# Kernel optimization log

Measured on AMD Instinct MI355X. Metric: run time of the kernel, lower is better.

## Reference

```python
import jax, jax.numpy as jnp
import numpy as np

N_NODES = 32768
N_EDGES = 131072
BATCH = 512
SEQ_LEN = 1000
VOCAB = 26  # vocab_size=25 + 1 padding row
EMB = 128


def _bn(x, g, b):
    # BatchNorm1d forward with batch statistics (training-mode math), eps=1e-5
    m = x.mean(0)
    v = x.var(0)
    return g * (x - m) * jax.lax.rsqrt(v + 1e-5) + b


def _gcn(x, src, dst, W, b, n):
    deg = 1.0 + jax.ops.segment_sum(jnp.ones(src.shape[0], x.dtype), dst, num_segments=n)
    dis = jax.lax.rsqrt(deg)
    xw = x @ W
    msg = xw[src] * (dis[src] * dis[dst])[:, None]
    agg = jax.ops.segment_sum(msg, dst, num_segments=n) + xw * (dis * dis)[:, None]
    return agg + b


def _conv1d(x, k, b, pad):
    # x: [B, C_in, L], k: [C_out, C_in, K]
    y = jax.lax.conv_general_dilated(x, k, (1,), [(pad, pad)],
                                     dimension_numbers=('NCH', 'OIH', 'NCH'))
    return y + b[None, :, None]


def setup_inputs() -> dict:
    key = jax.random.key(0)
    ks = jax.random.split(key, 32)
    f = lambda i, shape, s=0.1: (jax.random.normal(ks[i], shape, dtype=jnp.float32) * s)
    inp = {
        'x': jax.random.normal(ks[0], (N_NODES, 5), dtype=jnp.float32),
        'edge_index': jax.random.randint(ks[1], (2, N_EDGES), 0, N_NODES, dtype=jnp.int32),
        'batch': jnp.sort(jax.random.randint(ks[2], (N_NODES,), 0, BATCH, dtype=jnp.int32)),
        'protein_seq': jax.random.randint(ks[3], (BATCH, SEQ_LEN), 0, VOCAB, dtype=jnp.int32),
        # GCN weights
        'W1': f(4, (5, 64)), 'b1': f(5, (64,)),
        'g1': jnp.ones((64,)), 'bt1': jnp.zeros((64,)),
        'W2': f(6, (64, 128)), 'b2': f(7, (128,)),
        'g2': jnp.ones((128,)), 'bt2': jnp.zeros((128,)),
        'W3': f(8, (128, 128)), 'b3': f(9, (128,)),
        'g3': jnp.ones((128,)), 'bt3': jnp.zeros((128,)),
        # protein embedding (row 0 = padding_idx, zeroed)
        'emb': f(10, (VOCAB, EMB)).at[0].set(0.0),
        # protein convs
        'ck1': f(11, (32, 128, 4)), 'cb1': f(12, (32,)),
        'ck2': f(13, (64, 32, 6)), 'cb2': f(14, (64,)),
        'ck3': f(15, (96, 64, 8)), 'cb3': f(16, (96,)),
        'fw1': f(17, (224, 512)), 'fb1': f(18, (512,)),
        'fw2': f(19, (512, 256)), 'fb2': f(20, (256,)),
        'fw3': f(21, (256, 1)), 'fb3': f(22, (1,)),
    }
    return inp


def reference(x, edge_index, batch, protein_seq,
              W1, b1, g1, bt1, W2, b2, g2, bt2, W3, b3, g3, bt3,
              emb, ck1, cb1, ck2, cb2, ck3, cb3,
              fw1, fb1, fw2, fb2, fw3, fb3):
    src, dst = edge_index[0], edge_index[1]
    relu = jax.nn.relu
    # Drug GNN encoder
    h = relu(_bn(_gcn(x, src, dst, W1, b1, N_NODES), g1, bt1))
    h = relu(_bn(_gcn(h, src, dst, W2, b2, N_NODES), g2, bt2))
    h = relu(_bn(_gcn(h, src, dst, W3, b3, N_NODES), g3, bt3))
    cnt = jax.ops.segment_sum(jnp.ones(N_NODES, h.dtype), batch, num_segments=BATCH)
    drug_emb = jax.ops.segment_sum(h, batch, num_segments=BATCH) / jnp.maximum(cnt, 1.0)[:, None]
    # Protein CNN encoder
    e = emb[protein_seq]                    # [B, L, 128]
    p = jnp.transpose(e, (0, 2, 1))         # [B, 128, L]
    p = relu(_conv1d(p, ck1, cb1, 1))       # [B, 32, 999]
    p = relu(_conv1d(p, ck2, cb2, 2))       # [B, 64, 998]
    p = relu(_conv1d(p, ck3, cb3, 3))       # [B, 96, 997]
    prot_emb = p.max(axis=2)                # [B, 96]
    c = jnp.concatenate([drug_emb, prot_emb], axis=1)  # [B, 224]
    c = relu(c @ fw1 + fb1)
    c = relu(c @ fw2 + fb2)
    out = (c @ fw3 + fb3)[:, 0]             # [B]
    return out
```

## Files before the change

### kernel.cpp

```cpp
#include <hip/hip_runtime.h>

#define NN 32768
#define NE 131072
#define NB 512
#define SL 1000

using bf16x8 = __attribute__((ext_vector_type(8))) short;
using f32x4  = __attribute__((ext_vector_type(4))) float;

static __device__ __forceinline__ unsigned short f2b(float f) {
  union { float f; unsigned u; } x; x.f = f;
  unsigned r = x.u + 0x7fffu + ((x.u >> 16) & 1u);
  return (unsigned short)(r >> 16);
}

static __device__ __forceinline__ void bn_from_raw(float sum, float ssq, float g, float b,
                                                   float& sc, float& sh) {
  float m = sum / 32768.f;
  float v = ssq / 32768.f - m * m;
  sc = g * rsqrtf(v + 1e-5f);
  sh = b - m * sc;
}

__global__ void k_degprep(const int* __restrict__ dst, int* __restrict__ degi,
                          const float* __restrict__ emb, const float* __restrict__ ck1,
                          const float* __restrict__ ck2, const float* __restrict__ ck3,
                          unsigned short* __restrict__ emb_bf, unsigned short* __restrict__ wt1,
                          unsigned short* __restrict__ wt2, unsigned short* __restrict__ wt3,
                          float* __restrict__ e1) {
  int gid = blockIdx.x * 256 + threadIdx.x;
  atomicAdd(&degi[dst[gid]], 1);
  int idx = gid;
  if (idx < 3328) {
    emb_bf[idx] = f2b(emb[idx]);
  } else if (idx < 3328 + 16384) {
    int i = idx - 3328;
    int kt = i >> 12, co = (i >> 7) & 31, ci = i & 127;
    wt1[i] = f2b(ck1[co * 512 + ci * 4 + kt]);
  } else if (idx < 3328 + 16384 + 12288) {
    int i = idx - 3328 - 16384;
    int kt = i >> 11, co = (i >> 5) & 63, ci = i & 31;
    wt2[i] = f2b(ck2[co * 192 + ci * 6 + kt]);
  } else if (idx < 3328 + 16384 + 12288 + 49152) {
    int i = idx - 3328 - 16384 - 12288;
    int kt = i / 6144, co = (i >> 6) % 96, ci = i & 63;
    wt3[i] = f2b(ck3[co * 512 + ci * 8 + kt]);
  } else if (idx < 3328 + 16384 + 12288 + 49152 + 3328) {
    int i = idx - 81152;
    int t = i >> 7, kt = (i >> 5) & 3, co = i & 31;
    const float* er = emb + t * 128;
    float s = 0.f;
#pragma unroll 4
    for (int ci = 0; ci < 128; ++ci) s += er[ci] * ck1[co * 512 + ci * 4 + kt];
    e1[i] = s;
  }
}

__global__ void k_scan(const int* __restrict__ degi, int* __restrict__ base,
                       int* __restrict__ cursor, float* __restrict__ dis) {
  __shared__ int part[1024];
  int tid = threadIdx.x;
  int v[32];
  int s = 0;
  int lo = tid * 32;
#pragma unroll
  for (int i = 0; i < 32; ++i) { v[i] = degi[lo + i]; s += v[i]; }
  part[tid] = s;
  __syncthreads();
  for (int off = 1; off < 1024; off <<= 1) {
    int val = (tid >= off) ? part[tid - off] : 0;
    __syncthreads();
    part[tid] += val;
    __syncthreads();
  }
  int run = (tid > 0) ? part[tid - 1] : 0;
#pragma unroll
  for (int i = 0; i < 32; ++i) {
    base[lo + i] = run;
    cursor[lo + i] = run;
    dis[lo + i] = rsqrtf(1.0f + (float)v[i]);
    run += v[i];
  }
  if (tid == 1023) base[NN] = run;
}

__global__ void k_fill(const int* __restrict__ src, const int* __restrict__ dst,
                       int* __restrict__ cursor, unsigned short* __restrict__ csr_src, int E) {
  int e = blockIdx.x * 256 + threadIdx.x;
  if (e < E) {
    int d = dst[e];
    int pos = atomicAdd(&cursor[d], 1);
    csr_src[pos] = (unsigned short)src[e];
  }
}

__launch_bounds__(256)
__global__ void k_gfc1s(const float* __restrict__ x, const float* __restrict__ dis,
                        const int* __restrict__ base, const unsigned short* __restrict__ csr_src,
                        const float* __restrict__ W1, float* __restrict__ out,
                        float* __restrict__ st) {
  __shared__ float sW[5][64];
  __shared__ float a5[256][6];
  __shared__ float red[16][64];
  int tid = threadIdx.x;
  for (int i = tid; i < 320; i += 256) sW[i >> 6][i & 63] = W1[i];
  int n = blockIdx.x * 256 + tid;
  float dn = dis[n];
  float s2 = dn * dn;
  const float* xn = x + (long)n * 5;
  float a0 = xn[0] * s2, a1 = xn[1] * s2, a2 = xn[2] * s2, a3 = xn[3] * s2, a4 = xn[4] * s2;
  int b0 = base[n], b1 = base[n + 1];
  int sNext = (b0 < b1) ? csr_src[b0] : 0;
  for (int j = b0; j < b1; ++j) {
    int s = sNext;
    if (j + 1 < b1) sNext = csr_src[j + 1];
    float coef = dis[s] * dn;
    const float* xs = x + (long)s * 5;
    a0 += xs[0] * coef; a1 += xs[1] * coef; a2 += xs[2] * coef;
    a3 += xs[3] * coef; a4 += xs[4] * coef;
  }
  a5[tid][0] = a0; a5[tid][1] = a1; a5[tid][2] = a2; a5[tid][3] = a3; a5[tid][4] = a4;
  __syncthreads();
  int co = (tid & 15) * 4, strip = tid >> 4;
  float4 s4 = {0.f, 0.f, 0.f, 0.f}, ss4 = {0.f, 0.f, 0.f, 0.f};
  for (int i = 0; i < 16; ++i) {
    int nl = strip * 16 + i;
    long nn = (long)blockIdx.x * 256 + nl;
    float4 acc = {0.f, 0.f, 0.f, 0.f};
#pragma unroll
    for (int ci = 0; ci < 5; ++ci) {
      float av = a5[nl][ci];
      acc.x += av * sW[ci][co];     acc.y += av * sW[ci][co + 1];
      acc.z += av * sW[ci][co + 2]; acc.w += av * sW[ci][co + 3];
    }
    *(float4*)&out[nn * 64 + co] = acc;
    s4.x += acc.x; s4.y += acc.y; s4.z += acc.z; s4.w += acc.w;
    ss4.x += acc.x * acc.x; ss4.y += acc.y * acc.y;
    ss4.z += acc.z * acc.z; ss4.w += acc.w * acc.w;
  }
  *(float4*)&red[strip][co] = s4;
  __syncthreads();
  if (tid < 64) {
    float t = 0.f;
#pragma unroll
    for (int s = 0; s < 16; ++s) t += red[s][tid];
    atomicAdd(&st[tid], t);
  }
  __syncthreads();
  *(float4*)&red[strip][co] = ss4;
  __syncthreads();
  if (tid < 64) {
    float t = 0.f;
#pragma unroll
    for (int s = 0; s < 16; ++s) t += red[s][tid];
    atomicAdd(&st[64 + tid], t);
  }
}

template<int C>
__launch_bounds__(256)
__global__ void k_gbngather(const float* __restrict__ in, const float* __restrict__ dis,
                            const int* __restrict__ base, const unsigned short* __restrict__ csr_src,
                            const float* __restrict__ st, const float* __restrict__ g,
                            const float* __restrict__ bt, float* __restrict__ out) {
  constexpr int TPN = C / 4;
  int t = blockIdx.x * 256 + threadIdx.x;
  int n = t / TPN;
  int c = (t % TPN) * 4;
  float4 sum4 = *(const float4*)&st[c];
  float4 ssq4 = *(const float4*)&st[C + c];
  float4 gg = *(const float4*)&g[c];
  float4 bb = *(const float4*)&bt[c];
  float4 sc4, sh4;
  bn_from_raw(sum4.x, ssq4.x, gg.x, bb.x, sc4.x, sh4.x);
  bn_from_raw(sum4.y, ssq4.y, gg.y, bb.y, sc4.y, sh4.y);
  bn_from_raw(sum4.z, ssq4.z, gg.z, bb.z, sc4.z, sh4.z);
  bn_from_raw(sum4.w, ssq4.w, gg.w, bb.w, sc4.w, sh4.w);
  float dn = dis[n];
  float s2 = dn * dn;
  float4 a = *(const float4*)&in[(long)n * C + c];
  float4 acc;
  acc.x = fmaxf(a.x * sc4.x + sh4.x, 0.f) * s2;
  acc.y = fmaxf(a.y * sc4.y + sh4.y, 0.f) * s2;
  acc.z = fmaxf(a.z * sc4.z + sh4.z, 0.f) * s2;
  acc.w = fmaxf(a.w * sc4.w + sh4.w, 0.f) * s2;
  int b0 = base[n], b1 = base[n + 1];
  int sNext = (b0 < b1) ? csr_src[b0] : 0;
  for (int j = b0; j < b1; ++j) {
    int s = sNext;
    if (j + 1 < b1) sNext = csr_src[j + 1];
    float coef = dis[s] * dn;
    float4 vv = *(const float4*)&in[(long)s * C + c];
    acc.x += fmaxf(vv.x * sc4.x + sh4.x, 0.f) * coef;
    acc.y += fmaxf(vv.y * sc4.y + sh4.y, 0.f) * coef;
    acc.z += fmaxf(vv.z * sc4.z + sh4.z, 0.f) * coef;
    acc.w += fmaxf(vv.w * sc4.w + sh4.w, 0.f) * coef;
  }
  *(float4*)&out[(long)n * C + c] = acc;
}

template<int C_OUT, int K, int TN, bool RELU, bool BIAS, bool STATS>
__launch_bounds__(256)
__global__ void k_fc4(const float* __restrict__ in, const float* __restrict__ W,
                      const float* __restrict__ bias, float* __restrict__ out,
                      float* __restrict__ st, int N) {
  constexpr int CO4 = C_OUT / 4;
  constexpr int GPB = 256 / CO4;
  int g = blockIdx.x * GPB + threadIdx.x / CO4;
  long n0 = (long)g * TN;
  if (!STATS && n0 >= N) return;
  int co = (threadIdx.x % CO4) * 4;
  float4 acc[TN];
  float4 b4 = {0.f, 0.f, 0.f, 0.f};
  if (BIAS) b4 = *(const float4*)&bias[co];
#pragma unroll
  for (int t = 0; t < TN; ++t) acc[t] = b4;
  for (int ci = 0; ci < K; ci += 4) {
    float4 w0 = *(const float4*)&W[(long)(ci + 0) * C_OUT + co];
    float4 w1 = *(const float4*)&W[(long)(ci + 1) * C_OUT + co];
    float4 w2 = *(const float4*)&W[(long)(ci + 2) * C_OUT + co];
    float4 w3 = *(const float4*)&W[(long)(ci + 3) * C_OUT + co];
#pragma unroll
    for (int t = 0; t < TN; ++t) {
      float4 a = *(const float4*)&in[(n0 + t) * K + ci];
      acc[t].x += a.x * w0.x; acc[t].y += a.x * w0.y; acc[t].z += a.x * w0.z; acc[t].w += a.x * w0.w;
      acc[t].x += a.y * w1.x; acc[t].y += a.y * w1.y; acc[t].z += a.y * w1.z; acc[t].w += a.y * w1.w;
      acc[t].x += a.z * w2.x; acc[t].y += a.z * w2.y; acc[t].z += a.z * w2.z; acc[t].w += a.z * w2.w;
      acc[t].x += a.w * w3.x; acc[t].y += a.w * w3.y; acc[t].z += a.w * w3.z; acc[t].w += a.w * w3.w;
    }
  }
  float4 s4 = {0.f, 0.f, 0.f, 0.f}, ss4 = {0.f, 0.f, 0.f, 0.f};
#pragma unroll
  for (int t = 0; t < TN; ++t) {
    float4 o = acc[t];
    if (RELU) {
      o.x = fmaxf(o.x, 0.f); o.y = fmaxf(o.y, 0.f);
      o.z = fmaxf(o.z, 0.f); o.w = fmaxf(o.w, 0.f);
    }
    *(float4*)&out[(n0 + t) * C_OUT + co] = o;
    if (STATS) {
      s4.x += o.x; s4.y += o.y; s4.z += o.z; s4.w += o.w;
      ss4.x += o.x * o.x; ss4.y += o.y * o.y;
      ss4.z += o.z * o.z; ss4.w += o.w * o.w;
    }
  }
  if (STATS) {
    __shared__ float red2[GPB][C_OUT];
    int grp = threadIdx.x / CO4;
    *(float4*)&red2[grp][co] = s4;
    __syncthreads();
    if (threadIdx.x < C_OUT) {
      float t = 0.f;
#pragma unroll
      for (int s = 0; s < GPB; ++s) t += red2[s][threadIdx.x];
      atomicAdd(&st[threadIdx.x], t);
    }
    __syncthreads();
    *(float4*)&red2[grp][co] = ss4;
    __syncthreads();
    if (threadIdx.x < C_OUT) {
      float t = 0.f;
#pragma unroll
      for (int s = 0; s < GPB; ++s) t += red2[s][threadIdx.x];
      atomicAdd(&st[C_OUT + threadIdx.x], t);
    }
  }
}

__launch_bounds__(256)
__global__ void k_reg(const float* __restrict__ cbuf,
                      const float* __restrict__ fw1, const float* __restrict__ fb1,
                      const float* __restrict__ fw2, const float* __restrict__ fb2,
                      const float* __restrict__ fw3, const float* __restrict__ fb3,
                      float* __restrict__ out) {
  __shared__ float cin[224];
  __shared__ float h1[512];
  __shared__ float h2[256];
  __shared__ float red[4];
  int b = blockIdx.x, t = threadIdx.x;
  if (t < 224) cin[t] = cbuf[b * 224 + t];
  __syncthreads();
  {
    float a0 = fb1[t], a1 = fb1[t + 256];
    for (int ci = 0; ci < 224; ++ci) {
      float av = cin[ci];
      a0 += av * fw1[ci * 512 + t];
      a1 += av * fw1[ci * 512 + t + 256];
    }
    h1[t] = fmaxf(a0, 0.f);
    h1[t + 256] = fmaxf(a1, 0.f);
  }
  __syncthreads();
  {
    float a = fb2[t];
    for (int ci = 0; ci < 512; ++ci) a += h1[ci] * fw2[ci * 256 + t];
    h2[t] = fmaxf(a, 0.f);
  }
  __syncthreads();
  {
    float p = h2[t] * fw3[t];
#pragma unroll
    for (int off = 32; off > 0; off >>= 1) p += __shfl_down(p, off, 64);
    if ((t & 63) == 0) red[t >> 6] = p;
    __syncthreads();
    if (t == 0) out[b] = red[0] + red[1] + red[2] + red[3] + fb3[0];
  }
}

__launch_bounds__(256, 3)
__global__ void conv_mfma(const int* __restrict__ seq, const float* __restrict__ e1g,
                          const float* __restrict__ cb1,
                          const unsigned short* __restrict__ wt2g, const float* __restrict__ cb2,
                          const unsigned short* __restrict__ wt3g, const float* __restrict__ cb3,
                          const float* __restrict__ agg, const float* __restrict__ st3,
                          const float* __restrict__ g3, const float* __restrict__ bt3,
                          const int* __restrict__ batch, float* __restrict__ outmax) {
  __shared__ __align__(16) unsigned short s_w[12288];
  __shared__ __align__(16) unsigned short s_c1[4864];
  __shared__ __align__(16) unsigned short s_c2[9216];
  __shared__ int s_tok[152];
  __shared__ int s_max[96];

  int tid = threadIdx.x;
  int b = blockIdx.y;

  if (blockIdx.x == 8) {
    __shared__ int s_lo, s_hi;
    if (tid == 0) {
      int lo = 0, hi = NN;
      while (lo < hi) { int m = (lo + hi) >> 1; if (batch[m] < b) lo = m + 1; else hi = m; }
      s_lo = lo;
      hi = NN;
      while (lo < hi) { int m = (lo + hi) >> 1; if (batch[m] <= b) lo = m + 1; else hi = m; }
      s_hi = lo;
    }
    __syncthreads();
    if (tid < 128) {
      int lo = s_lo, hi = s_hi, c = tid;
      float sc, sh;
      bn_from_raw(st3[c], st3[128 + c], g3[c], bt3[c], sc, sh);
      float s = 0.f;
      for (int n = lo; n < hi; ++n) s += fmaxf(agg[(long)n * 128 + c] * sc + sh, 0.f);
      outmax[b * 224 + c] = s / fmaxf((float)(hi - lo), 1.0f);
    }
    return;
  }

  int t0 = blockIdx.x * 128;

  if (tid < 96) s_max[tid] = 0;
  if (tid < 152) {
    int p = t0 - 6 + tid;
    s_tok[tid] = (p >= 0 && p < SL) ? seq[b * SL + p] : 0;
  }
  if (tid < 128) ((int*)(s_c1 + 144 * 32))[tid] = 0;

  {
#pragma unroll
    for (int c = 0; c < 6; ++c) {
      int ch = c * 256 + tid;
      int row = ch >> 2;
      *(bf16x8*)&s_w[row * 32 + (((row ^ ch) & 3) << 3)] = *(const bf16x8*)(wt2g + ch * 8);
    }
  }
  __syncthreads();

  int lane = tid & 63, wave = tid >> 6;
  int l15 = lane & 15, quad = lane >> 4;

  {
    bool edge = (blockIdx.x == 0) || (blockIdx.x == 7);
#pragma unroll
    for (int pass = 0; pass < 2; ++pass) {
      int m = (pass == 0) ? (tid >> 1) : (128 + (tid >> 1));
      bool act = (pass == 0) || (tid < 32);
      if (act) {
        int co0 = (tid & 1) * 16;
        f32x4 a4[4];
#pragma unroll
        for (int q = 0; q < 4; ++q) a4[q] = *(const f32x4*)&cb1[co0 + q * 4];
#pragma unroll
        for (int kt = 0; kt < 4; ++kt) {
          const float* e = e1g + s_tok[m + kt] * 128 + kt * 32 + co0;
#pragma unroll
          for (int q = 0; q < 4; ++q) {
            f32x4 v = *(const f32x4*)&e[q * 4];
            a4[q][0] += v[0]; a4[q][1] += v[1]; a4[q][2] += v[2]; a4[q][3] += v[3];
          }
        }
        int l1 = t0 - 5 + m;
        bool ok = !edge || (l1 >= 0 && l1 < 999);
#pragma unroll
        for (int q = 0; q < 4; ++q) {
#pragma unroll
          for (int e2 = 0; e2 < 4; e2 += 2) {
            int co = co0 + q * 4 + e2;
            unsigned lo = ok ? (unsigned)f2b(fmaxf(a4[q][e2], 0.f)) : 0u;
            unsigned hi = ok ? (unsigned)f2b(fmaxf(a4[q][e2 + 1], 0.f)) : 0u;
            *(unsigned*)&s_c1[m * 32 + ((((co >> 3) ^ m) & 3) << 3) + (co & 7)] = lo | (hi << 16);
          }
        }
      }
    }
  }
  __syncthreads();

  {
    int mt0 = wave, mt1 = wave + 4;
    f32x4 acc[2][4];
#pragma unroll
    for (int nt = 0; nt < 4; ++nt) {
      float bv = cb2[nt * 16 + l15];
      acc[0][nt] = (f32x4){bv, bv, bv, bv};
      acc[1][nt] = (f32x4){bv, bv, bv, bv};
    }
    for (int kt = 0; kt < 6; ++kt) {
      int r0 = mt0 * 16 + l15 + kt, r1 = mt1 * 16 + l15 + kt;
      bf16x8 a0 = *(const bf16x8*)&s_c1[r0 * 32 + (((quad ^ r0) & 3) << 3)];
      bf16x8 a1 = *(const bf16x8*)&s_c1[r1 * 32 + (((quad ^ r1) & 3) << 3)];
#pragma unroll
      for (int nt = 0; nt < 4; ++nt) {
        int wr = kt * 64 + nt * 16 + l15;
        bf16x8 bf = *(const bf16x8*)&s_w[wr * 32 + (((quad ^ wr) & 3) << 3)];
        acc[0][nt] = __builtin_amdgcn_mfma_f32_16x16x32_bf16(a0, bf, acc[0][nt], 0, 0, 0);
        acc[1][nt] = __builtin_amdgcn_mfma_f32_16x16x32_bf16(a1, bf, acc[1][nt], 0, 0, 0);
      }
    }
#pragma unroll
    for (int mb = 0; mb < 2; ++mb) {
      int mt = mb ? mt1 : mt0;
#pragma unroll
      for (int nt = 0; nt < 4; ++nt) {
        int co = nt * 16 + l15;
#pragma unroll
        for (int r = 0; r < 4; ++r) {
          int m = mt * 16 + quad * 4 + r;
          int l2 = t0 - 3 + m;
          unsigned short hv = f2b(fmaxf(acc[mb][nt][r], 0.f));
          s_c2[m * 64 + ((((co >> 3) ^ m) & 7) << 3) + (co & 7)] = (l2 >= 0 && l2 < 998) ? hv : (unsigned short)0;
        }
      }
    }
    if (wave == 0) {
      f32x4 acc8[4];
#pragma unroll
      for (int nt = 0; nt < 4; ++nt) {
        float bv = cb2[nt * 16 + l15];
        acc8[nt] = (f32x4){bv, bv, bv, bv};
      }
      for (int kt = 0; kt < 6; ++kt) {
        int r0 = 128 + l15 + kt;
        bf16x8 a0 = *(const bf16x8*)&s_c1[r0 * 32 + (((quad ^ r0) & 3) << 3)];
#pragma unroll
        for (int nt = 0; nt < 4; ++nt) {
          int wr = kt * 64 + nt * 16 + l15;
          bf16x8 bf = *(const bf16x8*)&s_w[wr * 32 + (((quad ^ wr) & 3) << 3)];
          acc8[nt] = __builtin_amdgcn_mfma_f32_16x16x32_bf16(a0, bf, acc8[nt], 0, 0, 0);
        }
      }
#pragma unroll
      for (int nt = 0; nt < 4; ++nt) {
        int co = nt * 16 + l15;
#pragma unroll
        for (int r = 0; r < 4; ++r) {
          int m = 128 + quad * 4 + r;
          int l2 = t0 - 3 + m;
          unsigned short hv = f2b(fmaxf(acc8[nt][r], 0.f));
          s_c2[m * 64 + ((((co >> 3) ^ m) & 7) << 3) + (co & 7)] = (l2 >= 0 && l2 < 998) ? hv : (unsigned short)0;
        }
      }
    }
  }

  {
    bf16x8 w3t[3];
#pragma unroll
    for (int c = 0; c < 3; ++c) w3t[c] = *(const bf16x8*)(wt3g + (c * 256 + tid) * 8);
    __syncthreads();
#pragma unroll
    for (int c = 0; c < 3; ++c) {
      int ch = c * 256 + tid;
      int row = ch >> 3;
      *(bf16x8*)&s_w[row * 64 + (((row ^ ch) & 7) << 3)] = w3t[c];
    }
    __syncthreads();
  }

  {
    int mt0 = wave, mt1 = wave + 4;
    f32x4 acc[2][6];
#pragma unroll
    for (int nt = 0; nt < 6; ++nt) {
      float bv = cb3[nt * 16 + l15];
      acc[0][nt] = (f32x4){bv, bv, bv, bv};
      acc[1][nt] = (f32x4){bv, bv, bv, bv};
    }
    for (int kt = 0; kt < 8; ++kt) {
      bf16x8 w3t[3];
      if (kt < 7) {
#pragma unroll
        for (int c = 0; c < 3; ++c)
          w3t[c] = *(const bf16x8*)(wt3g + ((kt + 1) * 768 + c * 256 + tid) * 8);
      }
      int bo = (kt & 1) * 6144;
      int ra0 = mt0 * 16 + l15 + kt, ra1 = mt1 * 16 + l15 + kt;
#pragma unroll
      for (int cb = 0; cb < 2; ++cb) {
        bf16x8 a0 = *(const bf16x8*)&s_c2[ra0 * 64 + ((((cb * 4 + quad) ^ ra0) & 7) << 3)];
        bf16x8 a1 = *(const bf16x8*)&s_c2[ra1 * 64 + ((((cb * 4 + quad) ^ ra1) & 7) << 3)];
#pragma unroll
        for (int nt = 0; nt < 6; ++nt) {
          int wr = nt * 16 + l15;
          bf16x8 bf = *(const bf16x8*)&s_w[bo + wr * 64 + ((((cb * 4 + quad) ^ wr) & 7) << 3)];
          acc[0][nt] = __builtin_amdgcn_mfma_f32_16x16x32_bf16(a0, bf, acc[0][nt], 0, 0, 0);
          acc[1][nt] = __builtin_amdgcn_mfma_f32_16x16x32_bf16(a1, bf, acc[1][nt], 0, 0, 0);
        }
      }
      if (kt < 7) {
        int bo2 = 6144 - bo;
#pragma unroll
        for (int c = 0; c < 3; ++c) {
          int ch = c * 256 + tid;
          int row = ch >> 3;
          *(bf16x8*)&s_w[bo2 + row * 64 + (((row ^ ch) & 7) << 3)] = w3t[c];
        }
      }
      __syncthreads();
    }
#pragma unroll
    for (int nt = 0; nt < 6; ++nt) {
      int co = nt * 16 + l15;
      float mx = 0.f;
#pragma unroll
      for (int mb = 0; mb < 2; ++mb) {
        int mt = mb ? mt1 : mt0;
#pragma unroll
        for (int r = 0; r < 4; ++r) {
          int l3 = t0 + mt * 16 + quad * 4 + r;
          if (l3 < 997) mx = fmaxf(mx, acc[mb][nt][r]);
        }
      }
      atomicMax(&s_max[co], __float_as_int(mx));
    }
  }
  __syncthreads();
  if (tid < 96) atomicMax((int*)&outmax[b * 224 + 128 + tid], s_max[tid]);
}

extern "C" void kernel_launch(void* const* d_in, const int* in_sizes, int n_in,
                              void* d_out, int out_size, void* d_ws, size_t ws_size,
                              hipStream_t stream) {
  (void)in_sizes; (void)n_in; (void)out_size; (void)ws_size;
  const float* x = (const float*)d_in[0];
  const int* ei = (const int*)d_in[1];
  const int* batch = (const int*)d_in[2];
  const int* seq = (const int*)d_in[3];
  const float* W1 = (const float*)d_in[4];
  const float* g1 = (const float*)d_in[6];
  const float* bt1 = (const float*)d_in[7];
  const float* W2 = (const float*)d_in[8];
  const float* g2 = (const float*)d_in[10];
  const float* bt2 = (const float*)d_in[11];
  const float* W3 = (const float*)d_in[12];
  const float* g3 = (const float*)d_in[14];
  const float* bt3 = (const float*)d_in[15];
  const float* emb = (const float*)d_in[16];
  const float* ck1 = (const float*)d_in[17];
  const float* cb1 = (const float*)d_in[18];
  const float* ck2 = (const float*)d_in[19];
  const float* cb2 = (const float*)d_in[20];
  const float* ck3 = (const float*)d_in[21];
  const float* cb3 = (const float*)d_in[22];
  const float* fw1 = (const float*)d_in[23];
  const float* fb1 = (const float*)d_in[24];
  const float* fw2 = (const float*)d_in[25];
  const float* fb2 = (const float*)d_in[26];
  const float* fw3 = (const float*)d_in[27];
  const float* fb3 = (const float*)d_in[28];
  const int* src = ei;
  const int* dst = ei + NE;

  float* ws = (float*)d_ws;
  float* bufA = ws;
  float* bufB = ws + 4194304;
  float* dis = ws + 8388608;
  float* stats = ws + 8421376;
  float* cbuf = ws + 8422032;
  int* degi = (int*)(ws + 8536720);
  int* base = degi + NN;
  int* cursor = base + NN + 1;
  unsigned short* csr_src = (unsigned short*)(cursor + NN);
  unsigned short* emb_bf = (unsigned short*)(ws + 8700564);
  unsigned short* wt1 = emb_bf + 3328;
  unsigned short* wt2 = wt1 + 16384;
  unsigned short* wt3 = wt2 + 12288;
  float* e1 = ws + 8741140;
  float* out = (float*)d_out;

  hipMemsetAsync(stats, 0, (656 + 114688 + 32768) * sizeof(float), stream);

  k_degprep<<<NE / 256, 256, 0, stream>>>(dst, degi, emb, ck1, ck2, ck3, emb_bf, wt1, wt2, wt3, e1);
  k_scan<<<1, 1024, 0, stream>>>(degi, base, cursor, dis);
  k_fill<<<NE / 256, 256, 0, stream>>>(src, dst, cursor, csr_src, NE);

  k_gfc1s<<<NN / 256, 256, 0, stream>>>(x, dis, base, csr_src, W1, bufA, stats);
  k_gbngather<64><<<NN * 16 / 256, 256, 0, stream>>>(bufA, dis, base, csr_src, stats, g1, bt1, bufB);
  k_fc4<128, 64, 4, false, false, true><<<1024, 256, 0, stream>>>(bufB, W2, nullptr, bufA, stats + 128, NN);
  k_gbngather<128><<<NN * 32 / 256, 256, 0, stream>>>(bufA, dis, base, csr_src, stats + 128, g2, bt2, bufB);
  k_fc4<128, 128, 4, false, false, true><<<1024, 256, 0, stream>>>(bufB, W3, nullptr, bufA, stats + 384, NN);

  conv_mfma<<<dim3(9, NB), 256, 0, stream>>>(seq, e1, cb1, wt2, cb2, wt3, cb3,
                                             bufA, stats + 384, g3, bt3, batch, cbuf);

  k_reg<<<NB, 256, 0, stream>>>(cbuf, fw1, fb1, fw2, fb2, fw3, fb3, out);
}
```

Before: 408.3 us.

## Double sequence tile per block in fused protein conv kernel to cut halo and weight reloads

The fused conv kernel now gives each block 256 sequence positions instead of 128, so 4 tile blocks plus one pooling block per batch row replace 8 plus one. This halves the redundant halo recomputation and the per-block weight staging into LDS, and each wave reuses every loaded weight fragment across four M-tiles. In exchange, LDS use and accumulator registers per block roughly double, launch bounds drop from 3 to 2 blocks per CU, and the grid shrinks, which lowers occupancy and parallelism.

After: 413.2 us. No clear change (+1.2%).

```diff
diff --git a/kernel.cpp b/kernel.cpp
--- a/kernel.cpp
+++ b/kernel.cpp
@@ -307,7 +307,7 @@
   }
 }
 
-__launch_bounds__(256, 3)
+__launch_bounds__(256, 2)
 __global__ void conv_mfma(const int* __restrict__ seq, const float* __restrict__ e1g,
                           const float* __restrict__ cb1,
                           const unsigned short* __restrict__ wt2g, const float* __restrict__ cb2,
@@ -316,15 +316,15 @@
                           const float* __restrict__ g3, const float* __restrict__ bt3,
                           const int* __restrict__ batch, float* __restrict__ outmax) {
   __shared__ __align__(16) unsigned short s_w[12288];
-  __shared__ __align__(16) unsigned short s_c1[4864];
-  __shared__ __align__(16) unsigned short s_c2[9216];
-  __shared__ int s_tok[152];
+  __shared__ __align__(16) unsigned short s_c1[8960];
+  __shared__ __align__(16) unsigned short s_c2[17408];
+  __shared__ int s_tok[276];
   __shared__ int s_max[96];
 
   int tid = threadIdx.x;
   int b = blockIdx.y;
 
-  if (blockIdx.x == 8) {
+  if (blockIdx.x == 4) {
     __shared__ int s_lo, s_hi;
     if (tid == 0) {
       int lo = 0, hi = NN;
@@ -346,14 +346,19 @@
     return;
   }
 
-  int t0 = blockIdx.x * 128;
+  int t0 = blockIdx.x * 256;
 
   if (tid < 96) s_max[tid] = 0;
-  if (tid < 152) {
+  {
     int p = t0 - 6 + tid;
     s_tok[tid] = (p >= 0 && p < SL) ? seq[b * SL + p] : 0;
   }
-  if (tid < 128) ((int*)(s_c1 + 144 * 32))[tid] = 0;
+  if (tid < 20) {
+    int i = 256 + tid;
+    int p = t0 - 6 + i;
+    s_tok[i] = (p >= 0 && p < SL) ? seq[b * SL + p] : 0;
+  }
+  if (tid < 128) ((int*)(s_c1 + 272 * 32))[tid] = 0;
 
   {
 #pragma unroll
@@ -369,11 +374,11 @@
   int l15 = lane & 15, quad = lane >> 4;
 
   {
-    bool edge = (blockIdx.x == 0) || (blockIdx.x == 7);
-#pragma unroll
-    for (int pass = 0; pass < 2; ++pass) {
-      int m = (pass == 0) ? (tid >> 1) : (128 + (tid >> 1));
-      bool act = (pass == 0) || (tid < 32);
+    bool edge = (blockIdx.x == 0) || (blockIdx.x == 3);
+#pragma unroll
+    for (int pass = 0; pass < 3; ++pass) {
+      int m = pass * 128 + (tid >> 1);
+      bool act = (pass < 2) || (tid < 32);
       if (act) {
         int co0 = (tid & 1) * 16;
         f32x4 a4[4];
@@ -406,29 +411,41 @@
   __syncthreads();
 
   {
-    int mt0 = wave, mt1 = wave + 4;
-    f32x4 acc[2][4];
+    f32x4 acc[4][4];
+    f32x4 acc8[4];
 #pragma unroll
     for (int nt = 0; nt < 4; ++nt) {
       float bv = cb2[nt * 16 + l15];
-      acc[0][nt] = (f32x4){bv, bv, bv, bv};
-      acc[1][nt] = (f32x4){bv, bv, bv, bv};
+#pragma unroll
+      for (int j = 0; j < 4; ++j) acc[j][nt] = (f32x4){bv, bv, bv, bv};
+      acc8[nt] = (f32x4){bv, bv, bv, bv};
     }
     for (int kt = 0; kt < 6; ++kt) {
-      int r0 = mt0 * 16 + l15 + kt, r1 = mt1 * 16 + l15 + kt;
-      bf16x8 a0 = *(const bf16x8*)&s_c1[r0 * 32 + (((quad ^ r0) & 3) << 3)];
-      bf16x8 a1 = *(const bf16x8*)&s_c1[r1 * 32 + (((quad ^ r1) & 3) << 3)];
+      bf16x8 bfr[4];
 #pragma unroll
       for (int nt = 0; nt < 4; ++nt) {
         int wr = kt * 64 + nt * 16 + l15;
-        bf16x8 bf = *(const bf16x8*)&s_w[wr * 32 + (((quad ^ wr) & 3) << 3)];
-        acc[0][nt] = __builtin_amdgcn_mfma_f32_16x16x32_bf16(a0, bf, acc[0][nt], 0, 0, 0);
-        acc[1][nt] = __builtin_amdgcn_mfma_f32_16x16x32_bf16(a1, bf, acc[1][nt], 0, 0, 0);
-      }
-    }
-#pragma unroll
-    for (int mb = 0; mb < 2; ++mb) {
-      int mt = mb ? mt1 : mt0;
+        bfr[nt] = *(const bf16x8*)&s_w[wr * 32 + (((quad ^ wr) & 3) << 3)];
+      }
+#pragma unroll
+      for (int j = 0; j < 4; ++j) {
+        int r0 = (wave + 4 * j) * 16 + l15 + kt;
+        bf16x8 a0 = *(const bf16x8*)&s_c1[r0 * 32 + (((quad ^ r0) & 3) << 3)];
+#pragma unroll
+        for (int nt = 0; nt < 4; ++nt)
+          acc[j][nt] = __builtin_amdgcn_mfma_f32_16x16x32_bf16(a0, bfr[nt], acc[j][nt], 0, 0, 0);
+      }
+      if (wave == 0) {
+        int r8 = 256 + l15 + kt;
+        bf16x8 a8 = *(const bf16x8*)&s_c1[r8 * 32 + (((quad ^ r8) & 3) << 3)];
+#pragma unroll
+        for (int nt = 0; nt < 4; ++nt)
+          acc8[nt] = __builtin_amdgcn_mfma_f32_16x16x32_bf16(a8, bfr[nt], acc8[nt], 0, 0, 0);
+      }
+    }
+#pragma unroll
+    for (int j = 0; j < 4; ++j) {
+      int mt = wave + 4 * j;
 #pragma unroll
       for (int nt = 0; nt < 4; ++nt) {
         int co = nt * 16 + l15;
@@ -436,34 +453,18 @@
         for (int r = 0; r < 4; ++r) {
           int m = mt * 16 + quad * 4 + r;
           int l2 = t0 - 3 + m;
-          unsigned short hv = f2b(fmaxf(acc[mb][nt][r], 0.f));
+          unsigned short hv = f2b(fmaxf(acc[j][nt][r], 0.f));
           s_c2[m * 64 + ((((co >> 3) ^ m) & 7) << 3) + (co & 7)] = (l2 >= 0 && l2 < 998) ? hv : (unsigned short)0;
         }
       }
     }
     if (wave == 0) {
-      f32x4 acc8[4];
-#pragma unroll
-      for (int nt = 0; nt < 4; ++nt) {
-        float bv = cb2[nt * 16 + l15];
-        acc8[nt] = (f32x4){bv, bv, bv, bv};
-      }
-      for (int kt = 0; kt < 6; ++kt) {
-        int r0 = 128 + l15 + kt;
-        bf16x8 a0 = *(const bf16x8*)&s_c1[r0 * 32 + (((quad ^ r0) & 3) << 3)];
-#pragma unroll
-        for (int nt = 0; nt < 4; ++nt) {
-          int wr = kt * 64 + nt * 16 + l15;
-          bf16x8 bf = *(const bf16x8*)&s_w[wr * 32 + (((quad ^ wr) & 3) << 3)];
-          acc8[nt] = __builtin_amdgcn_mfma_f32_16x16x32_bf16(a0, bf, acc8[nt], 0, 0, 0);
-        }
-      }
 #pragma unroll
       for (int nt = 0; nt < 4; ++nt) {
         int co = nt * 16 + l15;
 #pragma unroll
         for (int r = 0; r < 4; ++r) {
-          int m = 128 + quad * 4 + r;
+          int m = 256 + quad * 4 + r;
           int l2 = t0 - 3 + m;
           unsigned short hv = f2b(fmaxf(acc8[nt][r], 0.f));
           s_c2[m * 64 + ((((co >> 3) ^ m) & 7) << 3) + (co & 7)] = (l2 >= 0 && l2 < 998) ? hv : (unsigned short)0;
@@ -487,13 +488,12 @@
   }
 
   {
-    int mt0 = wave, mt1 = wave + 4;
-    f32x4 acc[2][6];
+    f32x4 acc[4][6];
 #pragma unroll
     for (int nt = 0; nt < 6; ++nt) {
       float bv = cb3[nt * 16 + l15];
-      acc[0][nt] = (f32x4){bv, bv, bv, bv};
-      acc[1][nt] = (f32x4){bv, bv, bv, bv};
+#pragma unroll
+      for (int j = 0; j < 4; ++j) acc[j][nt] = (f32x4){bv, bv, bv, bv};
     }
     for (int kt = 0; kt < 8; ++kt) {
       bf16x8 w3t[3];
@@ -503,17 +503,21 @@
           w3t[c] = *(const bf16x8*)(wt3g + ((kt + 1) * 768 + c * 256 + tid) * 8);
       }
       int bo = (kt & 1) * 6144;
-      int ra0 = mt0 * 16 + l15 + kt, ra1 = mt1 * 16 + l15 + kt;
 #pragma unroll
       for (int cb = 0; cb < 2; ++cb) {
-        bf16x8 a0 = *(const bf16x8*)&s_c2[ra0 * 64 + ((((cb * 4 + quad) ^ ra0) & 7) << 3)];
-        bf16x8 a1 = *(const bf16x8*)&s_c2[ra1 * 64 + ((((cb * 4 + quad) ^ ra1) & 7) << 3)];
+        bf16x8 av[4];
+#pragma unroll
+        for (int j = 0; j < 4; ++j) {
+          int ra = (wave + 4 * j) * 16 + l15 + kt;
+          av[j] = *(const bf16x8*)&s_c2[ra * 64 + ((((cb * 4 + quad) ^ ra) & 7) << 3)];
+        }
 #pragma unroll
         for (int nt = 0; nt < 6; ++nt) {
           int wr = nt * 16 + l15;
           bf16x8 bf = *(const bf16x8*)&s_w[bo + wr * 64 + ((((cb * 4 + quad) ^ wr) & 7) << 3)];
-          acc[0][nt] = __builtin_amdgcn_mfma_f32_16x16x32_bf16(a0, bf, acc[0][nt], 0, 0, 0);
-          acc[1][nt] = __builtin_amdgcn_mfma_f32_16x16x32_bf16(a1, bf, acc[1][nt], 0, 0, 0);
+#pragma unroll
+          for (int j = 0; j < 4; ++j)
+            acc[j][nt] = __builtin_amdgcn_mfma_f32_16x16x32_bf16(av[j], bf, acc[j][nt], 0, 0, 0);
         }
       }
       if (kt < 7) {
@@ -532,12 +536,12 @@
       int co = nt * 16 + l15;
       float mx = 0.f;
 #pragma unroll
-      for (int mb = 0; mb < 2; ++mb) {
-        int mt = mb ? mt1 : mt0;
+      for (int j = 0; j < 4; ++j) {
+        int mt = wave + 4 * j;
 #pragma unroll
         for (int r = 0; r < 4; ++r) {
           int l3 = t0 + mt * 16 + quad * 4 + r;
-          if (l3 < 997) mx = fmaxf(mx, acc[mb][nt][r]);
+          if (l3 < 997) mx = fmaxf(mx, acc[j][nt][r]);
         }
       }
       atomicMax(&s_max[co], __float_as_int(mx));
@@ -609,7 +613,7 @@
   k_gbngather<128><<<NN * 32 / 256, 256, 0, stream>>>(bufA, dis, base, csr_src, stats + 128, g2, bt2, bufB);
   k_fc4<128, 128, 4, false, false, true><<<1024, 256, 0, stream>>>(bufB, W3, nullptr, bufA, stats + 384, NN);
 
-  conv_mfma<<<dim3(9, NB), 256, 0, stream>>>(seq, e1, cb1, wt2, cb2, wt3, cb3,
+  conv_mfma<<<dim3(5, NB), 256, 0, stream>>>(seq, e1, cb1, wt2, cb2, wt3, cb3,
                                              bufA, stats + 384, g3, bt3, batch, cbuf);
 
   k_reg<<<NB, 256, 0, stream>>>(cbuf, fw1, fb1, fw2, fb2, fw3, fb3, out);
```

## Co-schedule layer-2 GCN gather with protein conv blocks and move pooling to regressor

Applied to the files above, without the earlier changes.

The layer-2 normalized gather moves into extra blocks of the protein conv kernel (4096 conv blocks plus 4096 gather blocks in a single 1D grid), so the memory-bound graph gather and the MFMA conv run concurrently instead of back to back. Drug mean-pooling moves from the conv kernel into the regressor kernel, with per-graph node ranges computed by atomicMax in the fill kernel in place of per-block binary searches. Unused bf16 embedding and conv1 weight conversions are dropped. The cost is a larger, mixed-workload kernel whose register use and occupancy limits now also apply to the gather blocks, plus a serial pooling loop inside the regressor.

Result: slower. 429.1 us (+5.1%).

```diff
diff --git a/kernel.cpp b/kernel.cpp
--- a/kernel.cpp
+++ b/kernel.cpp
@@ -25,28 +25,21 @@
 __global__ void k_degprep(const int* __restrict__ dst, int* __restrict__ degi,
                           const float* __restrict__ emb, const float* __restrict__ ck1,
                           const float* __restrict__ ck2, const float* __restrict__ ck3,
-                          unsigned short* __restrict__ emb_bf, unsigned short* __restrict__ wt1,
                           unsigned short* __restrict__ wt2, unsigned short* __restrict__ wt3,
                           float* __restrict__ e1) {
   int gid = blockIdx.x * 256 + threadIdx.x;
   atomicAdd(&degi[dst[gid]], 1);
   int idx = gid;
-  if (idx < 3328) {
-    emb_bf[idx] = f2b(emb[idx]);
-  } else if (idx < 3328 + 16384) {
-    int i = idx - 3328;
-    int kt = i >> 12, co = (i >> 7) & 31, ci = i & 127;
-    wt1[i] = f2b(ck1[co * 512 + ci * 4 + kt]);
-  } else if (idx < 3328 + 16384 + 12288) {
-    int i = idx - 3328 - 16384;
+  if (idx < 12288) {
+    int i = idx;
     int kt = i >> 11, co = (i >> 5) & 63, ci = i & 31;
     wt2[i] = f2b(ck2[co * 192 + ci * 6 + kt]);
-  } else if (idx < 3328 + 16384 + 12288 + 49152) {
-    int i = idx - 3328 - 16384 - 12288;
+  } else if (idx < 12288 + 49152) {
+    int i = idx - 12288;
     int kt = i / 6144, co = (i >> 6) % 96, ci = i & 63;
     wt3[i] = f2b(ck3[co * 512 + ci * 8 + kt]);
-  } else if (idx < 3328 + 16384 + 12288 + 49152 + 3328) {
-    int i = idx - 81152;
+  } else if (idx < 12288 + 49152 + 3328) {
+    int i = idx - 61440;
     int t = i >> 7, kt = (i >> 5) & 3, co = i & 31;
     const float* er = emb + t * 128;
     float s = 0.f;
@@ -85,12 +78,19 @@
 }
 
 __global__ void k_fill(const int* __restrict__ src, const int* __restrict__ dst,
-                       int* __restrict__ cursor, unsigned short* __restrict__ csr_src, int E) {
+                       int* __restrict__ cursor, unsigned short* __restrict__ csr_src,
+                       const int* __restrict__ batch, int* __restrict__ blo,
+                       int* __restrict__ bhi, int E) {
   int e = blockIdx.x * 256 + threadIdx.x;
   if (e < E) {
     int d = dst[e];
     int pos = atomicAdd(&cursor[d], 1);
     csr_src[pos] = (unsigned short)src[e];
+  }
+  if (e < NN) {
+    int bb = batch[e];
+    atomicMax(&bhi[bb], e + 1);
+    atomicMax(&blo[bb], NN - e);
   }
 }
 
@@ -269,6 +269,9 @@
 
 __launch_bounds__(256)
 __global__ void k_reg(const float* __restrict__ cbuf,
+                      const int* __restrict__ blo, const int* __restrict__ bhi,
+                      const float* __restrict__ agg, const float* __restrict__ st3,
+                      const float* __restrict__ g3, const float* __restrict__ bt3,
                       const float* __restrict__ fw1, const float* __restrict__ fb1,
                       const float* __restrict__ fw2, const float* __restrict__ fb2,
                       const float* __restrict__ fw3, const float* __restrict__ fb3,
@@ -278,7 +281,16 @@
   __shared__ float h2[256];
   __shared__ float red[4];
   int b = blockIdx.x, t = threadIdx.x;
-  if (t < 224) cin[t] = cbuf[b * 224 + t];
+  if (t < 128) {
+    int lo = NN - blo[b], hi = bhi[b];
+    float sc, sh;
+    bn_from_raw(st3[t], st3[128 + t], g3[t], bt3[t], sc, sh);
+    float s = 0.f;
+    for (int n = lo; n < hi; ++n) s += fmaxf(agg[(long)n * 128 + t] * sc + sh, 0.f);
+    cin[t] = s / fmaxf((float)(hi - lo), 1.0f);
+  } else if (t < 224) {
+    cin[t] = cbuf[b * 224 + t];
+  }
   __syncthreads();
   {
     float a0 = fb1[t], a1 = fb1[t + 256];
@@ -312,9 +324,11 @@
                           const float* __restrict__ cb1,
                           const unsigned short* __restrict__ wt2g, const float* __restrict__ cb2,
                           const unsigned short* __restrict__ wt3g, const float* __restrict__ cb3,
-                          const float* __restrict__ agg, const float* __restrict__ st3,
-                          const float* __restrict__ g3, const float* __restrict__ bt3,
-                          const int* __restrict__ batch, float* __restrict__ outmax) {
+                          const float* __restrict__ gin, const float* __restrict__ dis,
+                          const int* __restrict__ base, const unsigned short* __restrict__ csr_src,
+                          const float* __restrict__ st2, const float* __restrict__ g2,
+                          const float* __restrict__ bt2, float* __restrict__ gout,
+                          float* __restrict__ outmax) {
   __shared__ __align__(16) unsigned short s_w[12288];
   __shared__ __align__(16) unsigned short s_c1[4864];
   __shared__ __align__(16) unsigned short s_c2[9216];
@@ -322,31 +336,47 @@
   __shared__ int s_max[96];
 
   int tid = threadIdx.x;
-  int b = blockIdx.y;
-
-  if (blockIdx.x == 8) {
-    __shared__ int s_lo, s_hi;
-    if (tid == 0) {
-      int lo = 0, hi = NN;
-      while (lo < hi) { int m = (lo + hi) >> 1; if (batch[m] < b) lo = m + 1; else hi = m; }
-      s_lo = lo;
-      hi = NN;
-      while (lo < hi) { int m = (lo + hi) >> 1; if (batch[m] <= b) lo = m + 1; else hi = m; }
-      s_hi = lo;
-    }
-    __syncthreads();
-    if (tid < 128) {
-      int lo = s_lo, hi = s_hi, c = tid;
-      float sc, sh;
-      bn_from_raw(st3[c], st3[128 + c], g3[c], bt3[c], sc, sh);
-      float s = 0.f;
-      for (int n = lo; n < hi; ++n) s += fmaxf(agg[(long)n * 128 + c] * sc + sh, 0.f);
-      outmax[b * 224 + c] = s / fmaxf((float)(hi - lo), 1.0f);
-    }
+
+  if (blockIdx.x >= 4096) {
+    int t = (blockIdx.x - 4096) * 256 + tid;
+    int n = t / 32;
+    int c = (t % 32) * 4;
+    float4 sum4 = *(const float4*)&st2[c];
+    float4 ssq4 = *(const float4*)&st2[128 + c];
+    float4 gg = *(const float4*)&g2[c];
+    float4 bb = *(const float4*)&bt2[c];
+    float4 sc4, sh4;
+    bn_from_raw(sum4.x, ssq4.x, gg.x, bb.x, sc4.x, sh4.x);
+    bn_from_raw(sum4.y, ssq4.y, gg.y, bb.y, sc4.y, sh4.y);
+    bn_from_raw(sum4.z, ssq4.z, gg.z, bb.z, sc4.z, sh4.z);
+    bn_from_raw(sum4.w, ssq4.w, gg.w, bb.w, sc4.w, sh4.w);
+    float dn = dis[n];
+    float s2 = dn * dn;
+    float4 a = *(const float4*)&gin[(long)n * 128 + c];
+    float4 acc;
+    acc.x = fmaxf(a.x * sc4.x + sh4.x, 0.f) * s2;
+    acc.y = fmaxf(a.y * sc4.y + sh4.y, 0.f) * s2;
+    acc.z = fmaxf(a.z * sc4.z + sh4.z, 0.f) * s2;
+    acc.w = fmaxf(a.w * sc4.w + sh4.w, 0.f) * s2;
+    int b0 = base[n], b1 = base[n + 1];
+    int sNext = (b0 < b1) ? csr_src[b0] : 0;
+    for (int j = b0; j < b1; ++j) {
+      int s = sNext;
+      if (j + 1 < b1) sNext = csr_src[j + 1];
+      float coef = dis[s] * dn;
+      float4 vv = *(const float4*)&gin[(long)s * 128 + c];
+      acc.x += fmaxf(vv.x * sc4.x + sh4.x, 0.f) * coef;
+      acc.y += fmaxf(vv.y * sc4.y + sh4.y, 0.f) * coef;
+      acc.z += fmaxf(vv.z * sc4.z + sh4.z, 0.f) * coef;
+      acc.w += fmaxf(vv.w * sc4.w + sh4.w, 0.f) * coef;
+    }
+    *(float4*)&gout[(long)n * 128 + c] = acc;
     return;
   }
 
-  int t0 = blockIdx.x * 128;
+  int tile = blockIdx.x >> 9;
+  int b = blockIdx.x & 511;
+  int t0 = tile * 128;
 
   if (tid < 96) s_max[tid] = 0;
   if (tid < 152) {
@@ -369,7 +399,7 @@
   int l15 = lane & 15, quad = lane >> 4;
 
   {
-    bool edge = (blockIdx.x == 0) || (blockIdx.x == 7);
+    bool edge = (tile == 0) || (tile == 7);
 #pragma unroll
     for (int pass = 0; pass < 2; ++pass) {
       int m = (pass == 0) ? (tid >> 1) : (128 + (tid >> 1));
@@ -595,22 +625,27 @@
   unsigned short* wt2 = wt1 + 16384;
   unsigned short* wt3 = wt2 + 12288;
   float* e1 = ws + 8741140;
+  int* blo = (int*)(ws + 8744468);
+  int* bhi = blo + 512;
   float* out = (float*)d_out;
 
   hipMemsetAsync(stats, 0, (656 + 114688 + 32768) * sizeof(float), stream);
-
-  k_degprep<<<NE / 256, 256, 0, stream>>>(dst, degi, emb, ck1, ck2, ck3, emb_bf, wt1, wt2, wt3, e1);
+  hipMemsetAsync(blo, 0, 1024 * sizeof(int), stream);
+
+  k_degprep<<<NE / 256, 256, 0, stream>>>(dst, degi, emb, ck1, ck2, ck3, wt2, wt3, e1);
   k_scan<<<1, 1024, 0, stream>>>(degi, base, cursor, dis);
-  k_fill<<<NE / 256, 256, 0, stream>>>(src, dst, cursor, csr_src, NE);
+  k_fill<<<NE / 256, 256, 0, stream>>>(src, dst, cursor, csr_src, batch, blo, bhi, NE);
 
   k_gfc1s<<<NN / 256, 256, 0, stream>>>(x, dis, base, csr_src, W1, bufA, stats);
   k_gbngather<64><<<NN * 16 / 256, 256, 0, stream>>>(bufA, dis, base, csr_src, stats, g1, bt1, bufB);
   k_fc4<128, 64, 4, false, false, true><<<1024, 256, 0, stream>>>(bufB, W2, nullptr, bufA, stats + 128, NN);
-  k_gbngather<128><<<NN * 32 / 256, 256, 0, stream>>>(bufA, dis, base, csr_src, stats + 128, g2, bt2, bufB);
+
+  conv_mfma<<<8192, 256, 0, stream>>>(seq, e1, cb1, wt2, cb2, wt3, cb3,
+                                      bufA, dis, base, csr_src, stats + 128, g2, bt2, bufB,
+                                      cbuf);
+
   k_fc4<128, 128, 4, false, false, true><<<1024, 256, 0, stream>>>(bufB, W3, nullptr, bufA, stats + 384, NN);
 
-  conv_mfma<<<dim3(9, NB), 256, 0, stream>>>(seq, e1, cb1, wt2, cb2, wt3, cb3,
-                                             bufA, stats + 384, g3, bt3, batch, cbuf);
-
-  k_reg<<<NB, 256, 0, stream>>>(cbuf, fw1, fb1, fw2, fb2, fw3, fb3, out);
-}
+  k_reg<<<NB, 256, 0, stream>>>(cbuf, blo, bhi, bufA, stats + 384, g3, bt3,
+                                fw1, fb1, fw2, fb2, fw3, fb3, out);
+}
```
